# Optimization experiments

Hardware: AMD Instinct MI355X
Metric: run time of the kernel (lower is better)

The kernel has to match this reference:

```python
import math
import jax, jax.numpy as jnp
import numpy as np

B, L, C, H = 2, 2048, 1024, 16
D = C // H


def new_gelu(x):
    return 0.5 * x * (1.0 + jnp.tanh(math.sqrt(2.0 / math.pi) * (x + 0.044715 * x ** 3)))


def layer_norm(x, w, b, eps=1e-5):
    mu = jnp.mean(x, axis=-1, keepdims=True)
    var = jnp.var(x, axis=-1, keepdims=True)
    return (x - mu) * jax.lax.rsqrt(var + eps) * w + b


def setup_inputs() -> dict:
    key = jax.random.key(0)
    ks = jax.random.split(key, 8)
    s = 0.02
    return {
        "x": jax.random.normal(ks[0], (B, L, C), dtype=jnp.float32),
        "ln1_w": jnp.ones((C,), jnp.float32),
        "ln1_b": jnp.zeros((C,), jnp.float32),
        "w_attn": jax.random.normal(ks[1], (C, 3 * C), dtype=jnp.float32) * s,
        "b_attn": jnp.zeros((3 * C,), jnp.float32),
        "w_proj": jax.random.normal(ks[2], (C, C), dtype=jnp.float32) * s,
        "b_proj": jnp.zeros((C,), jnp.float32),
        "ln2_w": jnp.ones((C,), jnp.float32),
        "ln2_b": jnp.zeros((C,), jnp.float32),
        "w_fc": jax.random.normal(ks[3], (C, 4 * C), dtype=jnp.float32) * s,
        "b_fc": jnp.zeros((4 * C,), jnp.float32),
        "w_fc2": jax.random.normal(ks[4], (4 * C, C), dtype=jnp.float32) * s,
        "b_fc2": jnp.zeros((C,), jnp.float32),
    }


def reference(x, ln1_w, ln1_b, w_attn, b_attn, w_proj, b_proj,
              ln2_w, ln2_b, w_fc, b_fc, w_fc2, b_fc2):
    # --- self-attention sublayer (pre-LN) ---
    h = layer_norm(x, ln1_w, ln1_b)
    qkv = h @ w_attn + b_attn                              # [B, L, 3C]
    q, k, v = jnp.split(qkv, 3, axis=-1)
    q = q.reshape(B, L, H, D)
    k = k.reshape(B, L, H, D)
    v = v.reshape(B, L, H, D)
    att = jnp.einsum("bqhd,bkhd->bhqk", q, k) * (1.0 / math.sqrt(D))
    causal = jnp.tril(jnp.ones((L, L), dtype=bool))
    att = jnp.where(causal[None, None], att, -jnp.inf)
    att = jax.nn.softmax(att, axis=-1)
    y = jnp.einsum("bhqk,bkhd->bqhd", att, v).reshape(B, L, C)
    y = y @ w_proj + b_proj
    x = x + y
    # --- MLP sublayer (pre-LN) ---
    h = layer_norm(x, ln2_w, ln2_b)
    h = new_gelu(h @ w_fc + b_fc)
    h = h @ w_fc2 + b_fc2
    return x + h
```

## Files before the change

kernel.cpp:

```cpp
#include <hip/hip_runtime.h>
#include <math.h>

#define B_ 2
#define L_ 2048
#define C_ 1024
#define H_ 16
#define M_ (B_*L_)

typedef short s16x8 __attribute__((ext_vector_type(8)));
typedef float f32x4 __attribute__((ext_vector_type(4)));

__device__ __forceinline__ unsigned short f2bf(float f) {
    unsigned int u = __float_as_uint(f);
    u += 0x7fffu + ((u >> 16) & 1u);
    return (unsigned short)(u >> 16);
}

__device__ __forceinline__ float fexp2(float x) {
#if __has_builtin(__builtin_amdgcn_exp2f)
    return __builtin_amdgcn_exp2f(x);
#else
    return exp2f(x);
#endif
}

__device__ __forceinline__ float frcp(float x) {
#if __has_builtin(__builtin_amdgcn_rcpf)
    return __builtin_amdgcn_rcpf(x);
#else
    return 1.0f / x;
#endif
}

__device__ __forceinline__ void gl_lds16(const void* g, void* l) {
    __builtin_amdgcn_global_load_lds(
        (const __attribute__((address_space(1))) void*)g,
        (__attribute__((address_space(3))) void*)l, 16, 0, 0);
}

__device__ __forceinline__ void ln_row(const float* __restrict__ x,
                                       const float* __restrict__ w,
                                       const float* __restrict__ b,
                                       unsigned short* __restrict__ out,
                                       int row, int t,
                                       float* red0, float* red1, float* mv) {
    float4 v = ((const float4*)(x + (size_t)row * C_))[t];
    float s  = v.x + v.y + v.z + v.w;
    float s2 = v.x*v.x + v.y*v.y + v.z*v.z + v.w*v.w;
    #pragma unroll
    for (int off = 32; off > 0; off >>= 1) {
        s  += __shfl_down(s, off);
        s2 += __shfl_down(s2, off);
    }
    int wave = t >> 6, lane = t & 63;
    if (lane == 0) { red0[wave] = s; red1[wave] = s2; }
    __syncthreads();
    if (t == 0) {
        float a = red0[0] + red0[1] + red0[2] + red0[3];
        float c = red1[0] + red1[1] + red1[2] + red1[3];
        float mean = a * (1.0f / C_);
        mv[0] = mean;
        mv[1] = rsqrtf(c * (1.0f / C_) - mean * mean + 1e-5f);
    }
    __syncthreads();
    float mean = mv[0], rstd = mv[1];
    float4 wv = ((const float4*)w)[t];
    float4 bv = ((const float4*)b)[t];
    ushort4 o;
    o.x = f2bf((v.x - mean) * rstd * wv.x + bv.x);
    o.y = f2bf((v.y - mean) * rstd * wv.y + bv.y);
    o.z = f2bf((v.z - mean) * rstd * wv.z + bv.z);
    o.w = f2bf((v.w - mean) * rstd * wv.w + bv.w);
    *(ushort4*)&out[(size_t)row * C_ + t * 4] = o;
}

__global__ __launch_bounds__(256) void ln_bf16(const float* __restrict__ x,
                                               const float* __restrict__ w,
                                               const float* __restrict__ b,
                                               unsigned short* __restrict__ out) {
    __shared__ float red0[4], red1[4], mv[2];
    ln_row(x, w, b, out, blockIdx.x, threadIdx.x, red0, red1, mv);
}

__global__ __launch_bounds__(256) void prep_kernel(
    const float* __restrict__ W0, unsigned short* __restrict__ T0,
    const float* __restrict__ W1, unsigned short* __restrict__ T1,
    const float* __restrict__ W2, unsigned short* __restrict__ T2,
    const float* __restrict__ W3, unsigned short* __restrict__ T3,
    const float* __restrict__ x, const float* __restrict__ lnw,
    const float* __restrict__ lnb, unsigned short* __restrict__ h) {
    __shared__ unsigned short Ts[32][33];
    __shared__ float red0[4], red1[4], mv[2];
    int id = blockIdx.x;
    int t = threadIdx.x;
    if (id >= 12288) {
        ln_row(x, lnw, lnb, h, id - 12288, t, red0, red1, mv);
        return;
    }
    const float* W; unsigned short* WT; int R, C, bx, by;
    if (id < 3072)      { W = W0; WT = T0; R = 1024; C = 3072; bx = id % 96;  by = id / 96; }
    else if (id < 4096) { W = W1; WT = T1; R = 1024; C = 1024; id -= 3072; bx = id & 31;  by = id >> 5; }
    else if (id < 8192) { W = W2; WT = T2; R = 1024; C = 4096; id -= 4096; bx = id & 127; by = id >> 7; }
    else                { W = W3; WT = T3; R = 4096; C = 1024; id -= 8192; bx = id & 31;  by = id >> 5; }
    int tx = t & 31, ty = t >> 5;
    int c0 = bx * 32, r0 = by * 32;
    #pragma unroll
    for (int k = 0; k < 4; ++k)
        Ts[ty + 8*k][tx] = f2bf(W[(size_t)(r0 + ty + 8*k) * C + c0 + tx]);
    __syncthreads();
    #pragma unroll
    for (int k = 0; k < 4; ++k)
        WT[(size_t)(c0 + ty + 8*k) * R + r0 + tx] = Ts[tx][ty + 8*k];
}

__device__ __forceinline__ float gelu_f(float x) {
    float u2 = 1.5957691216057308f * (x + 0.044715f * x * x * x);
    return x * frcp(1.0f + __expf(-u2));
}

template<int ACT, int OBF, int TN, int SC, int KS, int VT, int XS>
__global__ __launch_bounds__(256) void bgemm(const unsigned short* __restrict__ A,
                                             const unsigned short* __restrict__ BT,
                                             const float* __restrict__ bias,
                                             const float* __restrict__ res,
                                             void* __restrict__ Cout,
                                             unsigned short* __restrict__ VtP,
                                             int M, int N, int K) {
    __shared__ __align__(16) unsigned short As[128 * 64];
    __shared__ __align__(16) unsigned short Bs[TN * 64];
    const int t = threadIdx.x, w = t >> 6, quad = (t & 63) >> 4, ln15 = t & 15;
    constexpr int FJ = TN / 32;
    const int woff_m = (w >> 1) * 64, woff_n = (w & 1) * (TN / 2);
    int bxi = blockIdx.x, byi = blockIdx.y;
    if (XS) {
        int id = bxi + (int)gridDim.x * byi;
        int nt = (int)gridDim.x, xcd = id & 7, loc = id >> 3;
        int per = (nt + 7) >> 3;
        bxi = xcd * per + (loc % per);
        byi = loc / per;
        if (bxi >= nt) { bxi = id % nt; byi = id / nt; }
    }
    const int m0g = byi * 128, n0g = bxi * TN;
    f32x4 acc[4][FJ];
    #pragma unroll
    for (int fi = 0; fi < 4; ++fi)
        #pragma unroll
        for (int fj = 0; fj < FJ; ++fj)
            #pragma unroll
            for (int i = 0; i < 4; ++i) acc[fi][fj][i] = 0.0f;

    const int kbeg = (KS > 1) ? (int)blockIdx.z * (K / KS) : 0;
    const int kiters = ((KS > 1) ? K / KS : K) >> 6;

    const unsigned short* ap[4];
    #pragma unroll
    for (int j = 0; j < 4; ++j) {
        int c = j * 256 + t, row = c >> 3, u = (c & 7) ^ (row & 7);
        ap[j] = A + (size_t)(m0g + row) * K + kbeg + u * 8;
    }
    const unsigned short* bp[FJ];
    #pragma unroll
    for (int j = 0; j < FJ; ++j) {
        int c = j * 256 + t, row = c >> 3, u = (c & 7) ^ (row & 7);
        bp[j] = BT + (size_t)(n0g + row) * K + kbeg + u * 8;
    }

    for (int kk = 0; kk < kiters; ++kk) {
        __syncthreads();
        #pragma unroll
        for (int j = 0; j < 4; ++j) {
            gl_lds16(ap[j], As + (j * 256 + w * 64) * 8);
            ap[j] += 64;
        }
        #pragma unroll
        for (int j = 0; j < FJ; ++j) {
            gl_lds16(bp[j], Bs + (j * 256 + w * 64) * 8);
            bp[j] += 64;
        }
        __syncthreads();
        #pragma unroll
        for (int s = 0; s < 2; ++s) {
            s16x8 af[4], bfr[FJ];
            #pragma unroll
            for (int f = 0; f < 4; ++f) {
                int row = woff_m + f * 16 + ln15;
                af[f] = *(const s16x8*)&As[(row * 8 + ((s * 4 + quad) ^ (row & 7))) * 8];
            }
            #pragma unroll
            for (int f = 0; f < FJ; ++f) {
                int row = woff_n + f * 16 + ln15;
                bfr[f] = *(const s16x8*)&Bs[(row * 8 + ((s * 4 + quad) ^ (row & 7))) * 8];
            }
            #pragma unroll
            for (int fi = 0; fi < 4; ++fi)
                #pragma unroll
                for (int fj = 0; fj < FJ; ++fj)
                    acc[fi][fj] = __builtin_amdgcn_mfma_f32_16x16x32_bf16(af[fi], bfr[fj], acc[fi][fj], 0, 0, 0);
        }
    }

    const int colb = n0g + woff_n + ln15;
    if (KS > 1) {
        float* P = (float*)Cout + (size_t)blockIdx.z * M * N;
        #pragma unroll
        for (int fj = 0; fj < FJ; ++fj) {
            const int col = colb + fj * 16;
            #pragma unroll
            for (int fi = 0; fi < 4; ++fi) {
                const int row0 = m0g + woff_m + fi * 16 + quad * 4;
                #pragma unroll
                for (int i = 0; i < 4; ++i)
                    P[(size_t)(row0 + i) * N + col] = acc[fi][fj][i];
            }
        }
        return;
    }
    #pragma unroll
    for (int fj = 0; fj < FJ; ++fj) {
        const int col = colb + fj * 16;
        const float bv = bias[col];
        const float sc = (SC && col < C_) ? 0.18033688011112042f : 1.0f;
        if (VT && col >= 2 * C_) {
            const int vcol = col - 2 * C_;
            #pragma unroll
            for (int fi = 0; fi < 4; ++fi) {
                const int row0 = m0g + woff_m + fi * 16 + quad * 4;
                const int bb = row0 >> 11, l = row0 & (L_ - 1);
                ushort4 pk;
                pk.x = f2bf(acc[fi][fj][0] + bv);
                pk.y = f2bf(acc[fi][fj][1] + bv);
                pk.z = f2bf(acc[fi][fj][2] + bv);
                pk.w = f2bf(acc[fi][fj][3] + bv);
                *(ushort4*)&VtP[(size_t)(bb * 1024 + vcol) * L_ + l] = pk;
            }
        } else {
            #pragma unroll
            for (int fi = 0; fi < 4; ++fi) {
                const int row0 = m0g + woff_m + fi * 16 + quad * 4;
                #pragma unroll
                for (int i = 0; i < 4; ++i) {
                    float v = acc[fi][fj][i] + bv;
                    if (ACT) v = gelu_f(v);
                    if (SC) v *= sc;
                    size_t off = (size_t)(row0 + i) * N + col;
                    if (res != nullptr) v += res[off];
                    if (OBF) ((unsigned short*)Cout)[off] = f2bf(v);
                    else     ((float*)Cout)[off] = v;
                }
            }
        }
    }
}

__global__ __launch_bounds__(256) void combine_out(const float* __restrict__ p,
                                                   const float* __restrict__ bias,
                                                   const float* __restrict__ res,
                                                   float* __restrict__ out) {
    int idx = blockIdx.x * 256 + threadIdx.x;
    size_t off = (size_t)idx * 4;
    float4 a = *(const float4*)&p[off];
    float4 b = *(const float4*)&p[(size_t)M_ * C_ + off];
    float4 r = *(const float4*)&res[off];
    float4 bb = *(const float4*)&bias[off & (C_ - 1)];
    float4 o;
    o.x = a.x + b.x + r.x + bb.x;
    o.y = a.y + b.y + r.y + bb.y;
    o.z = a.z + b.z + r.z + bb.z;
    o.w = a.w + b.w + r.w + bb.w;
    *(float4*)&out[off] = o;
}

__global__ __launch_bounds__(256) void attn_kernel(const unsigned short* __restrict__ qkv,
                                                   const unsigned short* __restrict__ Vt,
                                                   unsigned short* __restrict__ y) {
    __shared__ __align__(16) unsigned short Qs[64 * 64];
    __shared__ __align__(16) unsigned short Ks[128 * 64];
    __shared__ __align__(16) unsigned short Vs[64 * 128];
    const int t = threadIdx.x, w = t >> 6, quad = (t & 63) >> 4, ln15 = t & 15;
    const int wq = w >> 1, wk = w & 1;
    const int id = blockIdx.x;
    const int bh = (id & 7) * 4 + ((id >> 3) & 3);
    const int qpair = id >> 5;
    const int b = bh >> 4, h = bh & 15;

    #pragma unroll 1
    for (int rep = 0; rep < 2; ++rep) {
        const int qt = rep == 0 ? (31 - qpair) : qpair;
        const int q0 = qt * 64;
        if (rep) __syncthreads();
        #pragma unroll
        for (int j = 0; j < 2; ++j) {
            int c = j * 256 + t;
            int row = c >> 3, u = (c & 7) ^ (row & 7);
            gl_lds16(qkv + (size_t)(b * L_ + q0 + row) * (3*C_) + h * 64 + u * 8,
                     Qs + (j * 256 + w * 64) * 8);
        }
        __syncthreads();
        s16x8 qb[2][2];
        #pragma unroll
        for (int qf = 0; qf < 2; ++qf) {
            int row = wq * 32 + qf * 16 + ln15;
            #pragma unroll
            for (int s = 0; s < 2; ++s)
                qb[qf][s] = *(const s16x8*)&Qs[row * 64 + (((s * 4 + quad)) ^ (row & 7)) * 8];
        }

        f32x4 O[4][2];
        float m_[2] = {-INFINITY, -INFINITY}, l_[2] = {0.0f, 0.0f};
        #pragma unroll
        for (int df = 0; df < 4; ++df)
            #pragma unroll
            for (int qf = 0; qf < 2; ++qf)
                #pragma unroll
                for (int i = 0; i < 4; ++i) O[df][qf][i] = 0.0f;

        const int nkt = (qt >> 1) + 1;
        for (int kt = 0; kt < nkt; ++kt) {
            __syncthreads();
            #pragma unroll
            for (int j = 0; j < 4; ++j) {
                int c = j * 256 + t;
                int row = c >> 3, u = (c & 7) ^ (row & 7);
                gl_lds16(qkv + (size_t)(b * L_ + kt * 128 + row) * (3*C_) + C_ + h * 64 + u * 8,
                         Ks + (j * 256 + w * 64) * 8);
            }
            #pragma unroll
            for (int j = 0; j < 4; ++j) {
                int c = j * 256 + t;
                int row = c >> 4, u = (c & 15) ^ (row & 15);
                gl_lds16(Vt + (size_t)(bh * 64 + row) * L_ + kt * 128 + u * 8,
                         Vs + (j * 256 + w * 64) * 8);
            }
            __syncthreads();

            f32x4 St[2][4];
            #pragma unroll
            for (int qf = 0; qf < 2; ++qf)
                #pragma unroll
                for (int kf = 0; kf < 4; ++kf)
                    #pragma unroll
                    for (int i = 0; i < 4; ++i) St[qf][kf][i] = 0.0f;
            #pragma unroll
            for (int s = 0; s < 2; ++s) {
                s16x8 ka[4];
                #pragma unroll
                for (int kf = 0; kf < 4; ++kf) {
                    int row = wk * 64 + kf * 16 + ln15;
                    ka[kf] = *(const s16x8*)&Ks[row * 64 + ((s * 4 + quad) ^ (row & 7)) * 8];
                }
                #pragma unroll
                for (int qf = 0; qf < 2; ++qf)
                    #pragma unroll
                    for (int kf = 0; kf < 4; ++kf)
                        St[qf][kf] = __builtin_amdgcn_mfma_f32_16x16x32_bf16(ka[kf], qb[qf][s], St[qf][kf], 0, 0, 0);
            }
            __syncthreads();

            unsigned short* Pw = Ks + w * 2048;
            const bool diag = (kt == nkt - 1);
            #pragma unroll
            for (int qf = 0; qf < 2; ++qf) {
                const int qg = q0 + wq * 32 + qf * 16 + ln15;
                float mt = -INFINITY;
                if (diag) {
                    #pragma unroll
                    for (int kf = 0; kf < 4; ++kf)
                        #pragma unroll
                        for (int i = 0; i < 4; ++i) {
                            int key = kt * 128 + wk * 64 + kf * 16 + quad * 4 + i;
                            float sv = St[qf][kf][i];
                            sv = (key > qg) ? -INFINITY : sv;
                            St[qf][kf][i] = sv;
                            mt = fmaxf(mt, sv);
                        }
                } else {
                    #pragma unroll
                    for (int kf = 0; kf < 4; ++kf)
                        #pragma unroll
                        for (int i = 0; i < 4; ++i) mt = fmaxf(mt, St[qf][kf][i]);
                }
                mt = fmaxf(mt, __shfl_xor(mt, 16));
                mt = fmaxf(mt, __shfl_xor(mt, 32));
                const float mn = fmaxf(m_[qf], mt);
                const float ms = (mn == -INFINITY) ? 0.0f : mn;
                const float alpha = fexp2(m_[qf] - ms);
                float rs = 0.0f;
                #pragma unroll
                for (int kf = 0; kf < 4; ++kf)
                    #pragma unroll
                    for (int i = 0; i < 4; ++i) {
                        float e = fexp2(St[qf][kf][i] - ms);
                        St[qf][kf][i] = e;
                        rs += e;
                    }
                rs += __shfl_xor(rs, 16);
                rs += __shfl_xor(rs, 32);
                l_[qf] = l_[qf] * alpha + rs;
                m_[qf] = mn;
                #pragma unroll
                for (int df = 0; df < 4; ++df) O[df][qf] *= alpha;
                #pragma unroll
                for (int kf = 0; kf < 4; ++kf) {
                    int row = qf * 16 + ln15;
                    int slot = (kf * 2 + (quad >> 1)) ^ (row & 7);
                    unsigned u0 = __float_as_uint(St[qf][kf][0]) + 0x8000u;
                    unsigned u1 = __float_as_uint(St[qf][kf][1]) + 0x8000u;
                    unsigned u2 = __float_as_uint(St[qf][kf][2]) + 0x8000u;
                    unsigned u3 = __float_as_uint(St[qf][kf][3]) + 0x8000u;
                    uint2 pk;
                    pk.x = __builtin_amdgcn_perm(u1, u0, 0x07060302u);
                    pk.y = __builtin_amdgcn_perm(u3, u2, 0x07060302u);
                    *(uint2*)&Pw[row * 64 + slot * 8 + (quad & 1) * 4] = pk;
                }
            }

            #pragma unroll
            for (int s2 = 0; s2 < 2; ++s2) {
                s16x8 pb[2], va[4];
                #pragma unroll
                for (int qf = 0; qf < 2; ++qf) {
                    int row = qf * 16 + ln15;
                    pb[qf] = *(const s16x8*)&Pw[row * 64 + ((s2 * 4 + quad) ^ (row & 7)) * 8];
                }
                #pragma unroll
                for (int df = 0; df < 4; ++df) {
                    int row = df * 16 + ln15;
                    int uu = wk * 8 + s2 * 4 + quad;
                    va[df] = *(const s16x8*)&Vs[row * 128 + (uu ^ (row & 15)) * 8];
                }
                #pragma unroll
                for (int df = 0; df < 4; ++df)
                    #pragma unroll
                    for (int qf = 0; qf < 2; ++qf)
                        O[df][qf] = __builtin_amdgcn_mfma_f32_16x16x32_bf16(va[df], pb[qf], O[df][qf], 0, 0, 0);
            }
        }

        __syncthreads();
        float* OB  = (float*)Vs;
        float* MLm = (float*)Qs;
        float* MLl = MLm + 64;
        if (wk == 1) {
            #pragma unroll
            for (int qf = 0; qf < 2; ++qf) {
                int rq = wq * 32 + qf * 16 + ln15;
                if (quad == 0) { MLm[rq] = m_[qf]; MLl[rq] = l_[qf]; }
                #pragma unroll
                for (int df = 0; df < 4; ++df) {
                    float4 o;
                    o.x = O[df][qf][0]; o.y = O[df][qf][1]; o.z = O[df][qf][2]; o.w = O[df][qf][3];
                    *(float4*)&OB[rq * 64 + df * 16 + quad * 4] = o;
                }
            }
        }
        __syncthreads();
        if (wk == 0) {
            #pragma unroll
            for (int qf = 0; qf < 2; ++qf) {
                const int rq = wq * 32 + qf * 16 + ln15;
                const float m1 = MLm[rq], l1 = MLl[rq];
                const float mF = fmaxf(m_[qf], m1);
                float e0 = fexp2(m_[qf] - mF);
                float e1 = (m1 == -INFINITY) ? 0.0f : fexp2(m1 - mF);
                const float linv = frcp(l_[qf] * e0 + l1 * e1);
                e0 *= linv; e1 *= linv;
                #pragma unroll
                for (int df = 0; df < 4; ++df) {
                    float4 o1 = *(const float4*)&OB[rq * 64 + df * 16 + quad * 4];
                    ushort4 yv;
                    yv.x = f2bf(O[df][qf][0] * e0 + o1.x * e1);
                    yv.y = f2bf(O[df][qf][1] * e0 + o1.y * e1);
                    yv.z = f2bf(O[df][qf][2] * e0 + o1.z * e1);
                    yv.w = f2bf(O[df][qf][3] * e0 + o1.w * e1);
                    *(ushort4*)&y[(size_t)(b * L_ + q0 + rq) * C_ + h * 64 + df * 16 + quad * 4] = yv;
                }
            }
        }
    }
}

#define MB(x) ((size_t)(x) << 20)

extern "C" void kernel_launch(void* const* d_in, const int* in_sizes, int n_in,
                              void* d_out, int out_size, void* d_ws, size_t ws_size,
                              hipStream_t stream) {
    const float* x      = (const float*)d_in[0];
    const float* ln1_w  = (const float*)d_in[1];
    const float* ln1_b  = (const float*)d_in[2];
    const float* w_attn = (const float*)d_in[3];
    const float* b_attn = (const float*)d_in[4];
    const float* w_proj = (const float*)d_in[5];
    const float* b_proj = (const float*)d_in[6];
    const float* ln2_w  = (const float*)d_in[7];
    const float* ln2_b  = (const float*)d_in[8];
    const float* w_fc   = (const float*)d_in[9];
    const float* b_fc   = (const float*)d_in[10];
    const float* w_fc2  = (const float*)d_in[11];
    const float* b_fc2  = (const float*)d_in[12];
    float* out = (float*)d_out;

    char* ws = (char*)d_ws;
    unsigned short* wT1  = (unsigned short*)(ws + MB(0));
    unsigned short* wT2  = (unsigned short*)(ws + MB(6));
    unsigned short* wT3  = (unsigned short*)(ws + MB(8));
    unsigned short* wT4  = (unsigned short*)(ws + MB(16));
    unsigned short* h_bf = (unsigned short*)(ws + MB(24));
    unsigned short* qkv  = (unsigned short*)(ws + MB(32));
    unsigned short* Vt   = (unsigned short*)(ws + MB(56));
    unsigned short* y_bf = (unsigned short*)(ws + MB(64));
    float*          x1   = (float*)(ws + MB(72));
    unsigned short* f_bf = (unsigned short*)(ws + MB(88));
    float*          part = (float*)(ws + MB(32));
    dim3 b256(256);

    prep_kernel<<<12288 + M_, b256, 0, stream>>>(w_attn, wT1, w_proj, wT2,
                                                 w_fc, wT3, w_fc2, wT4,
                                                 x, ln1_w, ln1_b, h_bf);
    bgemm<0,1,128,1,1,1,0><<<dim3(3*C_/128, M_/128), b256, 0, stream>>>(
        h_bf, wT1, b_attn, nullptr, qkv, Vt, M_, 3*C_, C_);
    attn_kernel<<<512, b256, 0, stream>>>(qkv, Vt, y_bf);
    bgemm<0,0,64,0,1,0,0><<<dim3(C_/64, M_/128), b256, 0, stream>>>(
        y_bf, wT2, b_proj, x, x1, nullptr, M_, C_, C_);
    ln_bf16<<<M_, b256, 0, stream>>>(x1, ln2_w, ln2_b, h_bf);
    bgemm<1,1,128,0,1,0,1><<<dim3(4*C_/128, M_/128), b256, 0, stream>>>(
        h_bf, wT3, b_fc, nullptr, f_bf, nullptr, M_, 4*C_, C_);
    bgemm<0,0,128,0,2,0,0><<<dim3(C_/128, M_/128, 2), b256, 0, stream>>>(
        f_bf, wT4, nullptr, nullptr, part, nullptr, M_, C_, 4*C_);
    combine_out<<<(M_*C_)/(4*256), b256, 0, stream>>>(part, b_fc2, x1, out);
}
```

Baseline: 359.1 us.

## Add 512-thread 256-wide GEMM kernel with async LDS pipeline for MLP layers

```diff
diff --git a/kernel.cpp b/kernel.cpp
--- a/kernel.cpp
+++ b/kernel.cpp
@@ -37,6 +37,11 @@
         (const __attribute__((address_space(1))) void*)g,
         (__attribute__((address_space(3))) void*)l, 16, 0, 0);
 }
+
+#define VMCNT8() asm volatile("s_waitcnt vmcnt(8)" ::: "memory")
+#define VMCNT6() asm volatile("s_waitcnt vmcnt(6)" ::: "memory")
+#define VMCNT0() asm volatile("s_waitcnt vmcnt(0)" ::: "memory")
+#define LGKM0()  asm volatile("s_waitcnt lgkmcnt(0)" ::: "memory")
 
 __device__ __forceinline__ void ln_row(const float* __restrict__ x,
                                        const float* __restrict__ w,
@@ -252,6 +257,177 @@
     }
 }
 
+template<int ACT, int OBF, int BM, int SC, int KS, int VT, int XS>
+__global__ __launch_bounds__(512) void bgemm2(const unsigned short* __restrict__ A,
+                                              const unsigned short* __restrict__ BT,
+                                              const float* __restrict__ bias,
+                                              const float* __restrict__ res,
+                                              void* __restrict__ Cout,
+                                              unsigned short* __restrict__ VtP,
+                                              int M, int N, int K) {
+    constexpr int MR = BM / 32;
+    constexpr int NR = 4;
+    constexpr int WM = BM / 2;
+    constexpr int RA = BM / 64;
+    constexpr int RB = 4;
+    __shared__ __align__(16) unsigned short As[2 * BM * 64];
+    __shared__ __align__(16) unsigned short Bs[2 * 256 * 64];
+    const int t = threadIdx.x, wv = t >> 6, quad = (t & 63) >> 4, ln15 = t & 15;
+    const int wm = wv >> 2, wn = wv & 3;
+    int bxi = blockIdx.x, byi = blockIdx.y;
+    if (XS) {
+        int id = bxi + (int)gridDim.x * byi;
+        int nt = (int)gridDim.x, xcd = id & 7, loc = id >> 3;
+        int per = nt >> 3;
+        bxi = xcd * per + (loc % per);
+        byi = loc / per;
+    }
+    const int m0g = byi * BM, n0g = bxi * 256;
+
+    f32x4 acc[MR][NR];
+    #pragma unroll
+    for (int mr = 0; mr < MR; ++mr)
+        #pragma unroll
+        for (int nr = 0; nr < NR; ++nr)
+            #pragma unroll
+            for (int i = 0; i < 4; ++i) acc[mr][nr][i] = 0.0f;
+
+    const int kbeg = (KS > 1) ? (int)blockIdx.z * (K / KS) : 0;
+    const int NT = ((KS > 1) ? K / KS : K) >> 6;
+
+    const unsigned short* ap[RA];
+    #pragma unroll
+    for (int j = 0; j < RA; ++j) {
+        int c = j * 512 + t, row = c >> 3, u = (t & 7) ^ (row & 7);
+        ap[j] = A + (size_t)(m0g + row) * K + kbeg + u * 8;
+    }
+    const unsigned short* bp[RB];
+    #pragma unroll
+    for (int j = 0; j < RB; ++j) {
+        int c = j * 512 + t, row = c >> 3, u = (t & 7) ^ (row & 7);
+        bp[j] = BT + (size_t)(n0g + row) * K + kbeg + u * 8;
+    }
+
+    auto STAGE = [&](int kt, int buf) {
+        unsigned short* Ad = As + buf * (BM * 64);
+        unsigned short* Bd = Bs + buf * (256 * 64);
+        #pragma unroll
+        for (int j = 0; j < RA; ++j)
+            gl_lds16(ap[j] + (size_t)kt * 64, Ad + (j * 512 + wv * 64) * 8);
+        #pragma unroll
+        for (int j = 0; j < RB; ++j)
+            gl_lds16(bp[j] + (size_t)kt * 64, Bd + (j * 512 + wv * 64) * 8);
+    };
+
+    STAGE(0, 0);
+    STAGE(1, 1);
+    if constexpr (RA + RB == 8) VMCNT8(); else VMCNT6();
+    __builtin_amdgcn_s_barrier();
+
+    int buf = 0;
+    for (int kt = 0; kt < NT; ++kt) {
+        const unsigned short* Ab = As + buf * (BM * 64);
+        const unsigned short* Bb = Bs + buf * (256 * 64);
+        s16x8 a0[MR], b0[NR], a1[MR], b1[NR];
+        #pragma unroll
+        for (int mr = 0; mr < MR; ++mr) {
+            int row = wm * WM + mr * 16 + ln15;
+            a0[mr] = *(const s16x8*)&Ab[(row * 8 + (quad ^ (row & 7))) * 8];
+        }
+        #pragma unroll
+        for (int nr = 0; nr < NR; ++nr) {
+            int row = wn * 64 + nr * 16 + ln15;
+            b0[nr] = *(const s16x8*)&Bb[(row * 8 + (quad ^ (row & 7))) * 8];
+        }
+        #pragma unroll
+        for (int mr = 0; mr < MR; ++mr)
+            #pragma unroll
+            for (int nr = 0; nr < NR; ++nr)
+                acc[mr][nr] = __builtin_amdgcn_mfma_f32_16x16x32_bf16(a0[mr], b0[nr], acc[mr][nr], 0, 0, 0);
+        #pragma unroll
+        for (int mr = 0; mr < MR; ++mr) {
+            int row = wm * WM + mr * 16 + ln15;
+            a1[mr] = *(const s16x8*)&Ab[(row * 8 + ((4 + quad) ^ (row & 7))) * 8];
+        }
+        #pragma unroll
+        for (int nr = 0; nr < NR; ++nr) {
+            int row = wn * 64 + nr * 16 + ln15;
+            b1[nr] = *(const s16x8*)&Bb[(row * 8 + ((4 + quad) ^ (row & 7))) * 8];
+        }
+        LGKM0();
+        __builtin_amdgcn_sched_barrier(0);
+        __builtin_amdgcn_s_barrier();
+        if (kt + 2 < NT) STAGE(kt + 2, buf);
+        __builtin_amdgcn_s_setprio(1);
+        #pragma unroll
+        for (int mr = 0; mr < MR; ++mr)
+            #pragma unroll
+            for (int nr = 0; nr < NR; ++nr)
+                acc[mr][nr] = __builtin_amdgcn_mfma_f32_16x16x32_bf16(a1[mr], b1[nr], acc[mr][nr], 0, 0, 0);
+        __builtin_amdgcn_s_setprio(0);
+        if (kt + 2 < NT) {
+            if constexpr (RA + RB == 8) VMCNT8(); else VMCNT6();
+            __builtin_amdgcn_s_barrier();
+        } else if (kt + 1 < NT) {
+            VMCNT0();
+            __builtin_amdgcn_s_barrier();
+        }
+        buf ^= 1;
+    }
+
+    const int colb = n0g + wn * 64 + ln15;
+    if (KS > 1) {
+        float* P = (float*)Cout + (size_t)blockIdx.z * M * N;
+        #pragma unroll
+        for (int nr = 0; nr < NR; ++nr) {
+            const int col = colb + nr * 16;
+            #pragma unroll
+            for (int mr = 0; mr < MR; ++mr) {
+                const int row0 = m0g + wm * WM + mr * 16 + quad * 4;
+                #pragma unroll
+                for (int i = 0; i < 4; ++i)
+                    P[(size_t)(row0 + i) * N + col] = acc[mr][nr][i];
+            }
+        }
+        return;
+    }
+    #pragma unroll
+    for (int nr = 0; nr < NR; ++nr) {
+        const int col = colb + nr * 16;
+        const float bv = bias[col];
+        const float sc = (SC && col < C_) ? 0.18033688011112042f : 1.0f;
+        if (VT && col >= 2 * C_) {
+            const int vcol = col - 2 * C_;
+            #pragma unroll
+            for (int mr = 0; mr < MR; ++mr) {
+                const int row0 = m0g + wm * WM + mr * 16 + quad * 4;
+                const int bb = row0 >> 11, l = row0 & (L_ - 1);
+                ushort4 pk;
+                pk.x = f2bf(acc[mr][nr][0] + bv);
+                pk.y = f2bf(acc[mr][nr][1] + bv);
+                pk.z = f2bf(acc[mr][nr][2] + bv);
+                pk.w = f2bf(acc[mr][nr][3] + bv);
+                *(ushort4*)&VtP[(size_t)(bb * 1024 + vcol) * L_ + l] = pk;
+            }
+        } else {
+            #pragma unroll
+            for (int mr = 0; mr < MR; ++mr) {
+                const int row0 = m0g + wm * WM + mr * 16 + quad * 4;
+                #pragma unroll
+                for (int i = 0; i < 4; ++i) {
+                    float v = acc[mr][nr][i] + bv;
+                    if (ACT) v = gelu_f(v);
+                    if (SC) v *= sc;
+                    size_t off = (size_t)(row0 + i) * N + col;
+                    if (res != nullptr) v += res[off];
+                    if (OBF) ((unsigned short*)Cout)[off] = f2bf(v);
+                    else     ((float*)Cout)[off] = v;
+                }
+            }
+        }
+    }
+}
+
 __global__ __launch_bounds__(256) void combine_out(const float* __restrict__ p,
                                                    const float* __restrict__ bias,
                                                    const float* __restrict__ res,
@@ -511,7 +687,7 @@
     float*          x1   = (float*)(ws + MB(72));
     unsigned short* f_bf = (unsigned short*)(ws + MB(88));
     float*          part = (float*)(ws + MB(32));
-    dim3 b256(256);
+    dim3 b256(256), b512(512);
 
     prep_kernel<<<12288 + M_, b256, 0, stream>>>(w_attn, wT1, w_proj, wT2,
                                                  w_fc, wT3, w_fc2, wT4,
@@ -522,9 +698,9 @@
     bgemm<0,0,64,0,1,0,0><<<dim3(C_/64, M_/128), b256, 0, stream>>>(
         y_bf, wT2, b_proj, x, x1, nullptr, M_, C_, C_);
     ln_bf16<<<M_, b256, 0, stream>>>(x1, ln2_w, ln2_b, h_bf);
-    bgemm<1,1,128,0,1,0,1><<<dim3(4*C_/128, M_/128), b256, 0, stream>>>(
+    bgemm2<1,1,256,0,1,0,1><<<dim3(4*C_/256, M_/256), b512, 0, stream>>>(
         h_bf, wT3, b_fc, nullptr, f_bf, nullptr, M_, 4*C_, C_);
-    bgemm<0,0,128,0,2,0,0><<<dim3(C_/128, M_/128, 2), b256, 0, stream>>>(
+    bgemm2<0,0,128,0,2,0,0><<<dim3(C_/256, M_/128, 2), b512, 0, stream>>>(
         f_bf, wT4, nullptr, nullptr, part, nullptr, M_, C_, 4*C_);
     combine_out<<<(M_*C_)/(4*256), b256, 0, stream>>>(part, b_fc2, x1, out);
 }
```

Result: faster. 336.6 us (-6.3%).
